# Kernel optimization log

Measured on AMD Instinct MI355X. Metric: run time of the kernel, lower is better.

The kernel has to match this reference:

```python
import jax, jax.numpy as jnp
import numpy as np

N_EMB = 1024
N_HEADS = 16


def setup_inputs() -> dict:
    key = jax.random.key(0)
    k1, k2, k3 = jax.random.split(key, 3)
    x = jax.random.normal(k1, (2, 2048, N_EMB), dtype=jnp.float32)
    # qkv linear params (torch Linear: y = x @ W.T + b; store W as [in, 3*in])
    W_qkv = jax.random.normal(k2, (N_EMB, 3 * N_EMB), dtype=jnp.float32) * (1.0 / np.sqrt(N_EMB))
    b_qkv = jax.random.normal(k3, (3 * N_EMB,), dtype=jnp.float32) * 0.02
    return {"x": x, "W_qkv": W_qkv, "b_qkv": b_qkv}


def reference(x, W_qkv, b_qkv):
    B, S, D = x.shape
    H = N_HEADS
    Dh = D // H
    qkv = x @ W_qkv + b_qkv                       # [B, S, 3D]
    q, k, v = jnp.split(qkv, 3, axis=-1)
    # [B, S, D] -> [B, H, S, Dh]
    q = q.reshape(B, S, H, Dh).transpose(0, 2, 1, 3)
    k = k.reshape(B, S, H, Dh).transpose(0, 2, 1, 3)
    v = v.reshape(B, S, H, Dh).transpose(0, 2, 1, 3)
    scores = jnp.einsum("bhqd,bhkd->bhqk", q, k) * (1.0 / np.sqrt(Dh))
    attn = jax.nn.softmax(scores, axis=-1)        # no causal mask in original
    out = jnp.einsum("bhqk,bhkd->bhqd", attn, v)  # [B, H, S, Dh]
    return out.transpose(0, 2, 1, 3).reshape(B, S, D)
```

## Files before the change

### kernel.cpp

```cpp
#include <hip/hip_runtime.h>

#define S_LEN 2048
#define D_EMB 1024
#define H_CNT 16
#define DHD   64
#define N_QKV 3072

typedef __attribute__((ext_vector_type(8))) short short8;
typedef __attribute__((ext_vector_type(4))) float f32x4;
typedef unsigned short u16;

__device__ __forceinline__ u16 f2bf(float f) {
  unsigned u = __float_as_uint(f);
  u += 0x7FFFu + ((u >> 16) & 1u);
  return (u16)(u >> 16);
}

__device__ __forceinline__ void gload16(const void* g, void* lds) {
  __builtin_amdgcn_global_load_lds(
      (const __attribute__((address_space(1))) void*)g,
      (__attribute__((address_space(3))) void*)lds, 16, 0, 0);
}

__global__ __launch_bounds__(256) void cvt_x_kern(const float* __restrict__ x,
                                                  u16* __restrict__ xb) {
  int i = blockIdx.x * 256 + threadIdx.x;
  float4 v = ((const float4*)x)[i];
  ((ushort4*)xb)[i] = make_ushort4(f2bf(v.x), f2bf(v.y), f2bf(v.z), f2bf(v.w));
}

__global__ __launch_bounds__(256) void cvt_wt_kern(const float* __restrict__ w,
                                                   u16* __restrict__ wt) {
  __shared__ u16 tile[64][65];
  const int ct = blockIdx.x, kt = blockIdx.y, t = threadIdx.x;
#pragma unroll
  for (int i = 0; i < 4; ++i) {
    int idx = t + i * 256;
    int kk = idx >> 4, c4 = (idx & 15) * 4;
    float4 v = *(const float4*)(w + (size_t)(kt * 64 + kk) * N_QKV + ct * 64 + c4);
    tile[kk][c4 + 0] = f2bf(v.x);
    tile[kk][c4 + 1] = f2bf(v.y);
    tile[kk][c4 + 2] = f2bf(v.z);
    tile[kk][c4 + 3] = f2bf(v.w);
  }
  __syncthreads();
#pragma unroll
  for (int i = 0; i < 2; ++i) {
    int id = t + i * 256;
    int c = id >> 3, k8 = (id & 7) * 8;
    short8 o;
#pragma unroll
    for (int j = 0; j < 8; ++j) o[j] = (short)tile[k8 + j][c];
    *(short8*)&wt[(size_t)(ct * 64 + c) * D_EMB + kt * 64 + k8] = o;
  }
}

__global__ __launch_bounds__(256) void qkv_gemm_kern(
    const u16* __restrict__ xb, const u16* __restrict__ wt,
    const float* __restrict__ bias,
    u16* __restrict__ qo, u16* __restrict__ ko, u16* __restrict__ vo) {
  __shared__ __align__(16) u16 As[128 * 64];
  __shared__ __align__(16) u16 Bs[128 * 64];
  const int t = threadIdx.x;
  const int w = t >> 6, l = t & 63, lr = l & 15, lg = l >> 4;
  const int wr = w >> 1, wc = w & 1;
  const int row0 = blockIdx.x * 128, col0 = blockIdx.y * 128;
  const int srow = l >> 3, scol = (l & 7) * 16;

  f32x4 acc[4][4];
#pragma unroll
  for (int m = 0; m < 4; ++m)
#pragma unroll
    for (int n = 0; n < 4; ++n) acc[m][n] = (f32x4){0.f, 0.f, 0.f, 0.f};

  for (int k0 = 0; k0 < D_EMB; k0 += 64) {
#pragma unroll
    for (int c = 0; c < 4; ++c) {
      int tr = w * 32 + c * 8 + srow;
      int sc = scol ^ ((tr & 7) << 4);
      gload16((const char*)xb + (size_t)(row0 + tr) * (D_EMB * 2) + k0 * 2 + sc,
              (char*)As + (w * 32 + c * 8) * 128);
      gload16((const char*)wt + (size_t)(col0 + tr) * (D_EMB * 2) + k0 * 2 + sc,
              (char*)Bs + (w * 32 + c * 8) * 128);
    }
    __syncthreads();
    short8 af[4][2], bfr[4][2];
#pragma unroll
    for (int m = 0; m < 4; ++m) {
      int ar = wr * 64 + m * 16 + lr;
#pragma unroll
      for (int kk = 0; kk < 2; ++kk)
        af[m][kk] = *(const short8*)&As[(ar << 6) + ((kk * 32 + lg * 8) ^ ((ar & 7) << 3))];
    }
#pragma unroll
    for (int n = 0; n < 4; ++n) {
      int br = wc * 64 + n * 16 + lr;
#pragma unroll
      for (int kk = 0; kk < 2; ++kk)
        bfr[n][kk] = *(const short8*)&Bs[(br << 6) + ((kk * 32 + lg * 8) ^ ((br & 7) << 3))];
    }
#pragma unroll
    for (int m = 0; m < 4; ++m)
#pragma unroll
      for (int n = 0; n < 4; ++n)
#pragma unroll
        for (int kk = 0; kk < 2; ++kk)
          acc[m][n] = __builtin_amdgcn_mfma_f32_16x16x32_bf16(af[m][kk], bfr[n][kk],
                                                              acc[m][n], 0, 0, 0);
    __syncthreads();
  }

  const int tsel = col0 >> 10;
  const int bb = row0 >> 11;
  const int s0 = (row0 & 2047) + wr * 64 + lg * 4;
  u16* dst = (tsel == 0) ? qo : (tsel == 1 ? ko : vo);
#pragma unroll
  for (int n = 0; n < 4; ++n) {
    int gc = col0 + wc * 64 + n * 16 + lr;
    float bn = bias[gc];
    int d = gc & 1023;
    int hh = d >> 6, dh = d & 63;
    size_t base_qk = ((size_t)(bb * H_CNT + hh) * S_LEN) * DHD + dh;
    size_t base_v  = ((size_t)(bb * H_CNT + hh) * DHD + dh) * S_LEN;
#pragma unroll
    for (int m = 0; m < 4; ++m)
#pragma unroll
      for (int r = 0; r < 4; ++r) {
        int srw = s0 + m * 16 + r;
        u16 hv = f2bf(acc[m][n][r] + bn);
        if (tsel < 2) dst[base_qk + (size_t)srw * DHD] = hv;
        else          dst[base_v + srw] = hv;
      }
  }
}

__global__ __launch_bounds__(256) void attn_kern(
    const u16* __restrict__ qp, const u16* __restrict__ kp,
    const u16* __restrict__ vtp, float* __restrict__ out) {
  __shared__ __align__(16) u16 Ks[64 * 64];
  __shared__ __align__(16) u16 Vs[64 * 64];
  __shared__ __align__(16) u16 Ps[4][16 * 64];
  const int t = threadIdx.x;
  const int w = t >> 6, l = t & 63, lr = l & 15, lg = l >> 4;
  const int qt = blockIdx.x, bh = blockIdx.y;
  const int b = bh >> 4, h = bh & 15;
  const int srow = l >> 3, scol = (l & 7) * 16;

  const u16* qbase = qp + ((size_t)bh * S_LEN + qt * 64 + w * 16) * DHD;
  short8 qf[2];
#pragma unroll
  for (int kk = 0; kk < 2; ++kk)
    qf[kk] = *(const short8*)(qbase + lr * DHD + kk * 32 + lg * 8);

  float mrun = -__builtin_inff(), lsum = 0.f;
  f32x4 oacc[4];
#pragma unroll
  for (int ct = 0; ct < 4; ++ct) oacc[ct] = (f32x4){0.f, 0.f, 0.f, 0.f};
  const float SC = 0.125f * 1.44269504f;

  const char* kt_g = (const char*)(kp + (size_t)bh * S_LEN * DHD);
  const char* vt_g = (const char*)(vtp + (size_t)bh * DHD * S_LEN);

  for (int kv0 = 0; kv0 < S_LEN; kv0 += 64) {
#pragma unroll
    for (int c = 0; c < 2; ++c) {
      int r8 = w * 16 + c * 8;
      int row = r8 + srow;
      int sc = scol ^ ((row & 7) << 4);
      gload16(kt_g + (size_t)(kv0 + row) * 128 + sc, (char*)Ks + r8 * 128);
      gload16(vt_g + (size_t)row * (S_LEN * 2) + kv0 * 2 + sc, (char*)Vs + r8 * 128);
    }
    __syncthreads();

    f32x4 st[4];
#pragma unroll
    for (int k2 = 0; k2 < 4; ++k2) st[k2] = (f32x4){0.f, 0.f, 0.f, 0.f};
#pragma unroll
    for (int kk = 0; kk < 2; ++kk)
#pragma unroll
      for (int k2 = 0; k2 < 4; ++k2) {
        int ar = k2 * 16 + lr;
        short8 a = *(const short8*)&Ks[(ar << 6) + ((kk * 32 + lg * 8) ^ ((ar & 7) << 3))];
        st[k2] = __builtin_amdgcn_mfma_f32_16x16x32_bf16(a, qf[kk], st[k2], 0, 0, 0);
      }

    float pv[4][4];
    float mx = -__builtin_inff();
#pragma unroll
    for (int k2 = 0; k2 < 4; ++k2)
#pragma unroll
      for (int r = 0; r < 4; ++r) {
        float v = st[k2][r] * SC;
        pv[k2][r] = v;
        mx = fmaxf(mx, v);
      }
    mx = fmaxf(mx, __shfl_xor(mx, 16, 64));
    mx = fmaxf(mx, __shfl_xor(mx, 32, 64));
    float mnew = fmaxf(mrun, mx);
    float fsc = exp2f(mrun - mnew);
    float rs = 0.f;
#pragma unroll
    for (int k2 = 0; k2 < 4; ++k2)
#pragma unroll
      for (int r = 0; r < 4; ++r) {
        float p = exp2f(pv[k2][r] - mnew);
        pv[k2][r] = p;
        rs += p;
      }
    rs += __shfl_xor(rs, 16, 64);
    rs += __shfl_xor(rs, 32, 64);
    lsum = lsum * fsc + rs;
    mrun = mnew;

    float fr[4];
#pragma unroll
    for (int r = 0; r < 4; ++r) fr[r] = __shfl(fsc, lg * 4 + r, 64);
#pragma unroll
    for (int ct = 0; ct < 4; ++ct)
#pragma unroll
      for (int r = 0; r < 4; ++r) oacc[ct][r] *= fr[r];

#pragma unroll
    for (int k2 = 0; k2 < 4; ++k2)
#pragma unroll
      for (int r = 0; r < 4; ++r) {
        int key = k2 * 16 + lg * 4 + r;
        Ps[w][(lr << 6) + (key ^ ((lr & 7) << 3))] = f2bf(pv[k2][r]);
      }

    short8 pa[2];
#pragma unroll
    for (int kk = 0; kk < 2; ++kk)
      pa[kk] = *(const short8*)&Ps[w][(lr << 6) + ((kk * 32 + lg * 8) ^ ((lr & 7) << 3))];
#pragma unroll
    for (int ct = 0; ct < 4; ++ct)
#pragma unroll
      for (int kk = 0; kk < 2; ++kk) {
        int br = ct * 16 + lr;
        short8 bv = *(const short8*)&Vs[(br << 6) + ((kk * 32 + lg * 8) ^ ((br & 7) << 3))];
        oacc[ct] = __builtin_amdgcn_mfma_f32_16x16x32_bf16(pa[kk], bv, oacc[ct], 0, 0, 0);
      }
    __syncthreads();
  }

  float inv = 1.0f / lsum;
  float invr[4];
#pragma unroll
  for (int r = 0; r < 4; ++r) invr[r] = __shfl(inv, lg * 4 + r, 64);
  const int qg0 = qt * 64 + w * 16 + lg * 4;
#pragma unroll
  for (int ct = 0; ct < 4; ++ct) {
    int col = h * 64 + ct * 16 + lr;
#pragma unroll
    for (int r = 0; r < 4; ++r)
      out[((size_t)b * S_LEN + qg0 + r) * D_EMB + col] = oacc[ct][r] * invr[r];
  }
}

extern "C" void kernel_launch(void* const* d_in, const int* in_sizes, int n_in,
                              void* d_out, int out_size, void* d_ws, size_t ws_size,
                              hipStream_t stream) {
  (void)in_sizes; (void)n_in; (void)out_size; (void)ws_size;
  const float* x  = (const float*)d_in[0];
  const float* Wq = (const float*)d_in[1];
  const float* bq = (const float*)d_in[2];
  float* out = (float*)d_out;
  char* ws = (char*)d_ws;
  u16* xb = (u16*)(ws);
  u16* wt = (u16*)(ws + (size_t)8  * 1024 * 1024);
  u16* qb = (u16*)(ws + (size_t)14 * 1024 * 1024);
  u16* kb = (u16*)(ws + (size_t)22 * 1024 * 1024);
  u16* vb = (u16*)(ws + (size_t)30 * 1024 * 1024);

  cvt_x_kern <<<4096, 256, 0, stream>>>(x, xb);
  cvt_wt_kern<<<dim3(48, 16), 256, 0, stream>>>(Wq, wt);
  qkv_gemm_kern<<<dim3(32, 24), 256, 0, stream>>>(xb, wt, bq, qb, kb, vb);
  attn_kern  <<<dim3(32, 32), 256, 0, stream>>>(qb, kb, vb, out);
}
```

Measured before the change: 221.4 us.

## Double-buffer attention K/V, lazy softmax rescale, fold scale into Q, vectorize GEMM epilogue

The attention kernel now double-buffers the K/V tiles in LDS, so the next tile's global-to-LDS load is issued before the current tile is computed. It also skips the running-max rescale of the accumulators unless the max grows by more than 8 in log2 units. The softmax scale is folded into Q inside the QKV GEMM epilogue. That epilogue now swaps operands for Q/K tiles and stages the outputs through LDS, so each thread writes 16-byte vectors instead of scattered 2-byte stores. Packed bf16 conversion instructions replace the manual rounding. The lazy rescale bounds exp2 values to at most 256, which costs some bf16 precision headroom for P.

```diff
diff --git a/kernel.cpp b/kernel.cpp
--- a/kernel.cpp
+++ b/kernel.cpp
@@ -16,6 +16,12 @@
   return (u16)(u >> 16);
 }
 
+__device__ __forceinline__ unsigned cvtpk(float lo, float hi) {
+  unsigned r;
+  asm("v_cvt_pk_bf16_f32 %0, %1, %2" : "=v"(r) : "v"(lo), "v"(hi));
+  return r;
+}
+
 __device__ __forceinline__ void gload16(const void* g, void* lds) {
   __builtin_amdgcn_global_load_lds(
       (const __attribute__((address_space(1))) void*)g,
@@ -26,7 +32,9 @@
                                                   u16* __restrict__ xb) {
   int i = blockIdx.x * 256 + threadIdx.x;
   float4 v = ((const float4*)x)[i];
-  ((ushort4*)xb)[i] = make_ushort4(f2bf(v.x), f2bf(v.y), f2bf(v.z), f2bf(v.w));
+  unsigned* o = (unsigned*)&((ushort4*)xb)[i];
+  o[0] = cvtpk(v.x, v.y);
+  o[1] = cvtpk(v.z, v.w);
 }
 
 __global__ __launch_bounds__(256) void cvt_wt_kern(const float* __restrict__ w,
@@ -59,13 +67,16 @@
     const u16* __restrict__ xb, const u16* __restrict__ wt,
     const float* __restrict__ bias,
     u16* __restrict__ qo, u16* __restrict__ ko, u16* __restrict__ vo) {
-  __shared__ __align__(16) u16 As[128 * 64];
-  __shared__ __align__(16) u16 Bs[128 * 64];
+  __shared__ __align__(16) u16 SM[128 * 128];
+  u16* As = SM;
+  u16* Bs = SM + 128 * 64;
   const int t = threadIdx.x;
   const int w = t >> 6, l = t & 63, lr = l & 15, lg = l >> 4;
   const int wr = w >> 1, wc = w & 1;
   const int row0 = blockIdx.x * 128, col0 = blockIdx.y * 128;
   const int srow = l >> 3, scol = (l & 7) * 16;
+  const int tsel = col0 >> 10;
+  const bool ctq = (tsel < 2);
 
   f32x4 acc[4][4];
 #pragma unroll
@@ -73,31 +84,37 @@
 #pragma unroll
     for (int n = 0; n < 4; ++n) acc[m][n] = (f32x4){0.f, 0.f, 0.f, 0.f};
 
-  for (int k0 = 0; k0 < D_EMB; k0 += 64) {
+  const int ldrow = w * 32;
+  for (int ki = 0; ki < 16; ++ki) {
+    int k0 = ki * 64;
 #pragma unroll
     for (int c = 0; c < 4; ++c) {
-      int tr = w * 32 + c * 8 + srow;
+      int tr = ldrow + c * 8 + srow;
       int sc = scol ^ ((tr & 7) << 4);
       gload16((const char*)xb + (size_t)(row0 + tr) * (D_EMB * 2) + k0 * 2 + sc,
-              (char*)As + (w * 32 + c * 8) * 128);
+              (char*)As + (ldrow + c * 8) * 128);
       gload16((const char*)wt + (size_t)(col0 + tr) * (D_EMB * 2) + k0 * 2 + sc,
-              (char*)Bs + (w * 32 + c * 8) * 128);
-    }
-    __syncthreads();
+              (char*)Bs + (ldrow + c * 8) * 128);
+    }
+    __syncthreads();
+    const u16* Ab = ctq ? Bs : As;
+    const u16* Bb = ctq ? As : Bs;
+    const int ar0 = ctq ? wc * 64 : wr * 64;
+    const int br0 = ctq ? wr * 64 : wc * 64;
     short8 af[4][2], bfr[4][2];
 #pragma unroll
     for (int m = 0; m < 4; ++m) {
-      int ar = wr * 64 + m * 16 + lr;
+      int ar = ar0 + m * 16 + lr;
 #pragma unroll
       for (int kk = 0; kk < 2; ++kk)
-        af[m][kk] = *(const short8*)&As[(ar << 6) + ((kk * 32 + lg * 8) ^ ((ar & 7) << 3))];
+        af[m][kk] = *(const short8*)&Ab[(ar << 6) + ((kk * 32 + lg * 8) ^ ((ar & 7) << 3))];
     }
 #pragma unroll
     for (int n = 0; n < 4; ++n) {
-      int br = wc * 64 + n * 16 + lr;
+      int br = br0 + n * 16 + lr;
 #pragma unroll
       for (int kk = 0; kk < 2; ++kk)
-        bfr[n][kk] = *(const short8*)&Bs[(br << 6) + ((kk * 32 + lg * 8) ^ ((br & 7) << 3))];
+        bfr[n][kk] = *(const short8*)&Bb[(br << 6) + ((kk * 32 + lg * 8) ^ ((br & 7) << 3))];
     }
 #pragma unroll
     for (int m = 0; m < 4; ++m)
@@ -110,35 +127,64 @@
     __syncthreads();
   }
 
-  const int tsel = col0 >> 10;
   const int bb = row0 >> 11;
-  const int s0 = (row0 & 2047) + wr * 64 + lg * 4;
-  u16* dst = (tsel == 0) ? qo : (tsel == 1 ? ko : vo);
-#pragma unroll
-  for (int n = 0; n < 4; ++n) {
-    int gc = col0 + wc * 64 + n * 16 + lr;
-    float bn = bias[gc];
-    int d = gc & 1023;
-    int hh = d >> 6, dh = d & 63;
-    size_t base_qk = ((size_t)(bb * H_CNT + hh) * S_LEN) * DHD + dh;
-    size_t base_v  = ((size_t)(bb * H_CNT + hh) * DHD + dh) * S_LEN;
-#pragma unroll
-    for (int m = 0; m < 4; ++m)
-#pragma unroll
-      for (int r = 0; r < 4; ++r) {
-        int srw = s0 + m * 16 + r;
-        u16 hv = f2bf(acc[m][n][r] + bn);
-        if (tsel < 2) dst[base_qk + (size_t)srw * DHD] = hv;
-        else          dst[base_v + srw] = hv;
+  if (ctq) {
+    const float scl = (tsel == 0) ? (0.125f * 1.44269504f) : 1.0f;
+    u16* dst = (tsel == 0) ? qo : ko;
+#pragma unroll
+    for (int m = 0; m < 4; ++m) {
+      int qc0 = wc * 64 + m * 16 + lg * 4;
+      float4 bn = *(const float4*)&bias[col0 + qc0];
+#pragma unroll
+      for (int n = 0; n < 4; ++n) {
+        int s = wr * 64 + n * 16 + lr;
+        uint2 pk;
+        pk.x = cvtpk((acc[m][n][0] + bn.x) * scl, (acc[m][n][1] + bn.y) * scl);
+        pk.y = cvtpk((acc[m][n][2] + bn.z) * scl, (acc[m][n][3] + bn.w) * scl);
+        *(uint2*)&SM[(s << 7) + (qc0 ^ ((s & 7) << 3))] = pk;
       }
+    }
+    __syncthreads();
+    const int c = t & 15, rl = t >> 4;
+#pragma unroll
+    for (int pass = 0; pass < 8; ++pass) {
+      int s = pass * 16 + rl;
+      short8 v = *(const short8*)&SM[(s << 7) + ((c ^ (s & 7)) << 3)];
+      int d = (col0 + c * 8) & 1023, hh = d >> 6, dh = d & 63;
+      *(short8*)(dst + ((size_t)(bb * H_CNT + hh) * S_LEN + (row0 & 2047) + s) * DHD + dh) = v;
+    }
+  } else {
+#pragma unroll
+    for (int n = 0; n < 4; ++n) {
+      int qc = wc * 64 + n * 16 + lr;
+      float bn = bias[col0 + qc];
+#pragma unroll
+      for (int m = 0; m < 4; ++m) {
+        int s0l = wr * 64 + m * 16 + lg * 4;
+        uint2 pk;
+        pk.x = cvtpk(acc[m][n][0] + bn, acc[m][n][1] + bn);
+        pk.y = cvtpk(acc[m][n][2] + bn, acc[m][n][3] + bn);
+        *(uint2*)&SM[(qc << 7) + (s0l ^ ((qc & 7) << 3))] = pk;
+      }
+    }
+    __syncthreads();
+    const int c = t & 15, rl = t >> 4;
+#pragma unroll
+    for (int pass = 0; pass < 8; ++pass) {
+      int qc = pass * 16 + rl;
+      short8 v = *(const short8*)&SM[(qc << 7) + ((c ^ (qc & 7)) << 3)];
+      int d = (col0 + qc) & 1023, hh = d >> 6, dh = d & 63;
+      *(short8*)(vo + ((size_t)(bb * H_CNT + hh) * DHD + dh) * S_LEN +
+                 (row0 & 2047) + c * 8) = v;
+    }
   }
 }
 
 __global__ __launch_bounds__(256) void attn_kern(
     const u16* __restrict__ qp, const u16* __restrict__ kp,
     const u16* __restrict__ vtp, float* __restrict__ out) {
-  __shared__ __align__(16) u16 Ks[64 * 64];
-  __shared__ __align__(16) u16 Vs[64 * 64];
+  __shared__ __align__(16) u16 Ks[2][64 * 64];
+  __shared__ __align__(16) u16 Vs[2][64 * 64];
   __shared__ __align__(16) u16 Ps[4][16 * 64];
   const int t = threadIdx.x;
   const int w = t >> 6, l = t & 63, lr = l & 15, lg = l >> 4;
@@ -156,21 +202,29 @@
   f32x4 oacc[4];
 #pragma unroll
   for (int ct = 0; ct < 4; ++ct) oacc[ct] = (f32x4){0.f, 0.f, 0.f, 0.f};
-  const float SC = 0.125f * 1.44269504f;
 
   const char* kt_g = (const char*)(kp + (size_t)bh * S_LEN * DHD);
   const char* vt_g = (const char*)(vtp + (size_t)bh * DHD * S_LEN);
 
-  for (int kv0 = 0; kv0 < S_LEN; kv0 += 64) {
-#pragma unroll
-    for (int c = 0; c < 2; ++c) {
-      int r8 = w * 16 + c * 8;
-      int row = r8 + srow;
-      int sc = scol ^ ((row & 7) << 4);
-      gload16(kt_g + (size_t)(kv0 + row) * 128 + sc, (char*)Ks + r8 * 128);
-      gload16(vt_g + (size_t)row * (S_LEN * 2) + kv0 * 2 + sc, (char*)Vs + r8 * 128);
-    }
-    __syncthreads();
+#define ATTN_STAGE(it, buf)                                                     \
+  {                                                                             \
+    int kv0 = (it) * 64;                                                        \
+    _Pragma("unroll") for (int c = 0; c < 2; ++c) {                             \
+      int r8 = w * 16 + c * 8;                                                  \
+      int row = r8 + srow;                                                      \
+      int sc = scol ^ ((row & 7) << 4);                                         \
+      gload16(kt_g + (size_t)(kv0 + row) * 128 + sc, (char*)Ks[buf] + r8 * 128);\
+      gload16(vt_g + (size_t)row * (S_LEN * 2) + kv0 * 2 + sc,                  \
+              (char*)Vs[buf] + r8 * 128);                                       \
+    }                                                                           \
+  }
+
+  ATTN_STAGE(0, 0)
+  __syncthreads();
+
+  for (int it = 0; it < S_LEN / 64; ++it) {
+    int cur = it & 1;
+    if (it < S_LEN / 64 - 1) ATTN_STAGE(it + 1, cur ^ 1)
 
     f32x4 st[4];
 #pragma unroll
@@ -180,53 +234,45 @@
 #pragma unroll
       for (int k2 = 0; k2 < 4; ++k2) {
         int ar = k2 * 16 + lr;
-        short8 a = *(const short8*)&Ks[(ar << 6) + ((kk * 32 + lg * 8) ^ ((ar & 7) << 3))];
+        short8 a = *(const short8*)&Ks[cur][(ar << 6) +
+                                           ((kk * 32 + lg * 8) ^ ((ar & 7) << 3))];
         st[k2] = __builtin_amdgcn_mfma_f32_16x16x32_bf16(a, qf[kk], st[k2], 0, 0, 0);
       }
 
-    float pv[4][4];
     float mx = -__builtin_inff();
 #pragma unroll
     for (int k2 = 0; k2 < 4; ++k2)
 #pragma unroll
-      for (int r = 0; r < 4; ++r) {
-        float v = st[k2][r] * SC;
-        pv[k2][r] = v;
-        mx = fmaxf(mx, v);
-      }
+      for (int r = 0; r < 4; ++r) mx = fmaxf(mx, st[k2][r]);
     mx = fmaxf(mx, __shfl_xor(mx, 16, 64));
     mx = fmaxf(mx, __shfl_xor(mx, 32, 64));
-    float mnew = fmaxf(mrun, mx);
-    float fsc = exp2f(mrun - mnew);
+    if (!__all(mx - mrun <= 8.0f)) {
+      float mnew = fmaxf(mrun, mx);
+      float fsc = exp2f(mrun - mnew);
+      float fr[4];
+#pragma unroll
+      for (int r = 0; r < 4; ++r) fr[r] = __shfl(fsc, lg * 4 + r, 64);
+#pragma unroll
+      for (int ct = 0; ct < 4; ++ct)
+#pragma unroll
+        for (int r = 0; r < 4; ++r) oacc[ct][r] *= fr[r];
+      lsum *= fsc;
+      mrun = mnew;
+    }
     float rs = 0.f;
 #pragma unroll
-    for (int k2 = 0; k2 < 4; ++k2)
-#pragma unroll
-      for (int r = 0; r < 4; ++r) {
-        float p = exp2f(pv[k2][r] - mnew);
-        pv[k2][r] = p;
-        rs += p;
-      }
+    for (int k2 = 0; k2 < 4; ++k2) {
+      float p0 = exp2f(st[k2][0] - mrun), p1 = exp2f(st[k2][1] - mrun);
+      float p2 = exp2f(st[k2][2] - mrun), p3 = exp2f(st[k2][3] - mrun);
+      rs += (p0 + p1) + (p2 + p3);
+      int key0 = k2 * 16 + lg * 4;
+      int e = key0 ^ ((lr & 7) << 3);
+      *(unsigned*)&Ps[w][(lr << 6) + e + 0] = cvtpk(p0, p1);
+      *(unsigned*)&Ps[w][(lr << 6) + e + 2] = cvtpk(p2, p3);
+    }
     rs += __shfl_xor(rs, 16, 64);
     rs += __shfl_xor(rs, 32, 64);
-    lsum = lsum * fsc + rs;
-    mrun = mnew;
-
-    float fr[4];
-#pragma unroll
-    for (int r = 0; r < 4; ++r) fr[r] = __shfl(fsc, lg * 4 + r, 64);
-#pragma unroll
-    for (int ct = 0; ct < 4; ++ct)
-#pragma unroll
-      for (int r = 0; r < 4; ++r) oacc[ct][r] *= fr[r];
-
-#pragma unroll
-    for (int k2 = 0; k2 < 4; ++k2)
-#pragma unroll
-      for (int r = 0; r < 4; ++r) {
-        int key = k2 * 16 + lg * 4 + r;
-        Ps[w][(lr << 6) + (key ^ ((lr & 7) << 3))] = f2bf(pv[k2][r]);
-      }
+    lsum += rs;
 
     short8 pa[2];
 #pragma unroll
@@ -237,7 +283,8 @@
 #pragma unroll
       for (int kk = 0; kk < 2; ++kk) {
         int br = ct * 16 + lr;
-        short8 bv = *(const short8*)&Vs[(br << 6) + ((kk * 32 + lg * 8) ^ ((br & 7) << 3))];
+        short8 bv = *(const short8*)&Vs[cur][(br << 6) +
+                                            ((kk * 32 + lg * 8) ^ ((br & 7) << 3))];
         oacc[ct] = __builtin_amdgcn_mfma_f32_16x16x32_bf16(pa[kk], bv, oacc[ct], 0, 0, 0);
       }
     __syncthreads();
```

Measured after the change: 194.5 us. -12.1%, faster.
